# Optimization experiments

Hardware: AMD Instinct MI355X
Metric: run time of the kernel (lower is better)

The kernel has to match this reference:

```python
import jax, jax.numpy as jnp
import numpy as np

HEADS = 16
DIM_HEAD = 64
SEG = 512        # segment_len (block-diagonal window)
P = 16           # num persistent memory tokens


def rmsnorm(x, g, eps=1e-6):
    var = jnp.mean(x * x, axis=-1, keepdims=True)
    return x * jax.lax.rsqrt(var + eps) * g


def setup_inputs() -> dict:
    key = jax.random.key(0)
    ks = jax.random.split(key, 6)
    B, S, D = 2, 4096, 1024
    inner = HEADS * DIM_HEAD
    return {
        "x": jax.random.normal(ks[0], (B, S, D), jnp.float32),
        "gamma": jnp.ones((D,), jnp.float32),
        "w_qkv": jax.random.normal(ks[1], (D, inner * 3), jnp.float32) * (D ** -0.5),
        "w_out": jax.random.normal(ks[2], (inner, D), jnp.float32) * (inner ** -0.5),
        "pm_k": jax.random.normal(ks[3], (HEADS, P, DIM_HEAD), jnp.float32) * 0.02,
        "pm_v": jax.random.normal(ks[4], (HEADS, P, DIM_HEAD), jnp.float32) * 0.02,
    }


def reference(x, gamma, w_qkv, w_out, pm_k, pm_v):
    # SegmentedAttention forward (MAC block-diagonal causal + persistent memory)
    B, S, D = x.shape
    pad = (-S) % SEG
    Sp = S + pad
    nw = Sp // SEG

    h = rmsnorm(x, gamma)
    qkv = h @ w_qkv                              # [B, S, 3*inner]
    q, k, v = jnp.split(qkv, 3, axis=-1)

    def fold(t):
        # pad and fold segments into batch: b (w n) (h d) -> b w h n d
        t = jnp.pad(t, ((0, 0), (0, pad), (0, 0)))
        t = t.reshape(B, nw, SEG, HEADS, DIM_HEAD)
        return t.transpose(0, 1, 3, 2, 4)        # [B, W, H, SEG, Dh]

    q, k, v = fold(q), fold(k), fold(v)

    # persistent memory tokens prepended to every segment's k/v
    pmk = jnp.broadcast_to(pm_k, (B, nw, HEADS, P, DIM_HEAD))
    pmv = jnp.broadcast_to(pm_v, (B, nw, HEADS, P, DIM_HEAD))
    k = jnp.concatenate([pmk, k], axis=3)        # [B, W, H, P+SEG, Dh]
    v = jnp.concatenate([pmv, v], axis=3)

    scale = DIM_HEAD ** -0.5
    sim = jnp.einsum('bwhid,bwhjd->bwhij', q, k) * scale  # [B,W,H,SEG,P+SEG]

    # mask: persistent mem always visible; within-segment causal (block
    # diagonality is implicit from folding segments into batch)
    qi = jnp.arange(SEG)[:, None]
    kj = jnp.arange(SEG + P)[None, :] - P
    mask = (kj < 0) | (qi >= kj)
    sim = jnp.where(mask, sim, -jnp.inf)

    attn = jax.nn.softmax(sim, axis=-1)
    out = jnp.einsum('bwhij,bwhjd->bwhid', attn, v)       # [B,W,H,SEG,Dh]
    out = out.transpose(0, 1, 3, 2, 4).reshape(B, Sp, HEADS * DIM_HEAD)
    out = out[:, :S]
    return out @ w_out
```

## Files before the change

kernel.cpp:

```cpp
#include <hip/hip_runtime.h>

typedef __attribute__((ext_vector_type(8))) short short8;
typedef __attribute__((ext_vector_type(4))) float float4v;

#define SEG 512
#define PMEM 16
#define NKEY 528

__device__ __forceinline__ float b2f(unsigned int u) {
    union { unsigned int i; float f; } v; v.i = u << 16; return v.f;
}
__device__ __forceinline__ unsigned short f2b(float f) {
    union { float f; unsigned int i; } v; v.f = f;
    unsigned int b = v.i;
    return (unsigned short)((b + 0x7FFFu + ((b >> 16) & 1u)) >> 16);
}

__device__ __forceinline__ void async_ld16(const unsigned short* g, unsigned short* l) {
    __builtin_amdgcn_global_load_lds(
        (const __attribute__((address_space(1))) void*)g,
        (__attribute__((address_space(3))) void*)l,
        16, 0, 0);
}

__global__ void detect_k(const unsigned short* __restrict__ g, int* __restrict__ flag) {
    if (threadIdx.x == 0) {
        int cnt = 0;
        for (int i = 0; i < 64; ++i) cnt += (g[2 * i] == 0x3F80u) ? 1 : 0;
        *flag = (cnt > 48) ? 1 : 0;
    }
}

__global__ void transpose_k(const void* __restrict__ in,
                            unsigned short* __restrict__ out, int R, int C,
                            const int* __restrict__ flagp) {
    __shared__ unsigned short t[32][33];
    int f = flagp[0];
    const unsigned short* in16 = (const unsigned short*)in;
    const float* in32 = (const float*)in;
    int bx = blockIdx.x * 32, by = blockIdx.y * 32;
    int tx = threadIdx.x, ty = threadIdx.y;
    #pragma unroll
    for (int j = 0; j < 32; j += 8) {
        long idx = (long)(by + ty + j) * C + bx + tx;
        t[ty + j][tx] = f ? in16[idx] : f2b(in32[idx]);
    }
    __syncthreads();
    #pragma unroll
    for (int j = 0; j < 32; j += 8)
        out[(long)(bx + ty + j) * R + by + tx] = t[tx][ty + j];
}

__global__ __launch_bounds__(256) void rmsnorm_k(
    const void* __restrict__ xv_, const void* __restrict__ gv_,
    unsigned short* __restrict__ h, const int* __restrict__ flagp) {
    __shared__ float wsum[4];
    int f = flagp[0];
    long row = blockIdx.x;
    int tid = threadIdx.x;
    float f0, f1, f2, f3, g0, g1, g2, g3;
    if (f) {
        const unsigned short* x = (const unsigned short*)xv_;
        const unsigned short* g = (const unsigned short*)gv_;
        uint2 xv = *(const uint2*)(x + row * 1024 + tid * 4);
        f0 = b2f(xv.x & 0xffffu); f1 = b2f(xv.x >> 16);
        f2 = b2f(xv.y & 0xffffu); f3 = b2f(xv.y >> 16);
        uint2 gv = *(const uint2*)(g + tid * 4);
        g0 = b2f(gv.x & 0xffffu); g1 = b2f(gv.x >> 16);
        g2 = b2f(gv.y & 0xffffu); g3 = b2f(gv.y >> 16);
    } else {
        const float* x = (const float*)xv_;
        const float* g = (const float*)gv_;
        float4 xv = *(const float4*)(x + row * 1024 + tid * 4);
        f0 = xv.x; f1 = xv.y; f2 = xv.z; f3 = xv.w;
        float4 gv = *(const float4*)(g + tid * 4);
        g0 = gv.x; g1 = gv.y; g2 = gv.z; g3 = gv.w;
    }
    float ss = f0 * f0 + f1 * f1 + f2 * f2 + f3 * f3;
    #pragma unroll
    for (int off = 1; off < 64; off <<= 1) ss += __shfl_xor(ss, off, 64);
    int lane = tid & 63, wv = tid >> 6;
    if (lane == 0) wsum[wv] = ss;
    __syncthreads();
    float tot = wsum[0] + wsum[1] + wsum[2] + wsum[3];
    float sc = rsqrtf(tot * (1.0f / 1024.0f) + 1e-6f);
    uint2 o;
    o.x = (unsigned int)f2b(f0 * sc * g0) | ((unsigned int)f2b(f1 * sc * g1) << 16);
    o.y = (unsigned int)f2b(f2 * sc * g2) | ((unsigned int)f2b(f3 * sc * g3) << 16);
    *(uint2*)(h + row * 1024 + tid * 4) = o;
}

__global__ __launch_bounds__(256) void gemm_bt(
    const unsigned short* __restrict__ A, const unsigned short* __restrict__ Bt,
    void* __restrict__ Cv, int M, int N, int K,
    const int* __restrict__ flagp, int out_mode) {
    __shared__ unsigned short As[128 * 32];
    __shared__ unsigned short Bs[128 * 32];
    int out_bf16 = out_mode == 0 ? 1 : flagp[0];
    int tid = threadIdx.x;
    int lane = tid & 63, wv = tid >> 6;
    int l15 = lane & 15, quad = lane >> 4;
    int wm = (wv >> 1) * 64, wn = (wv & 1) * 64;
    long m0 = (long)blockIdx.y * 128;
    long n0 = (long)blockIdx.x * 128;

    float4v acc[4][4];
    #pragma unroll
    for (int i = 0; i < 4; ++i)
        #pragma unroll
        for (int j = 0; j < 4; ++j) acc[i][j] = (float4v){0.f, 0.f, 0.f, 0.f};

    int r0 = tid >> 2;
    int cc = (tid & 3) * 8;
    const unsigned short* Ap = A + (m0 + r0) * K + cc;
    const unsigned short* Bp = Bt + (n0 + r0) * K + cc;
    unsigned short* As0 = As + tid * 8;
    unsigned short* As1 = As + 2048 + tid * 8;
    unsigned short* Bs0 = Bs + tid * 8;
    unsigned short* Bs1 = Bs + 2048 + tid * 8;

    for (int k0 = 0; k0 < K; k0 += 32) {
        async_ld16(Ap + k0, As0);
        async_ld16(Ap + 64 * K + k0, As1);
        async_ld16(Bp + k0, Bs0);
        async_ld16(Bp + 64 * K + k0, Bs1);
        __syncthreads();
        short8 af[4], bfr[4];
        #pragma unroll
        for (int mt = 0; mt < 4; ++mt)
            af[mt] = *(const short8*)&As[(wm + mt * 16 + l15) * 32 + quad * 8];
        #pragma unroll
        for (int nt = 0; nt < 4; ++nt)
            bfr[nt] = *(const short8*)&Bs[(wn + nt * 16 + l15) * 32 + quad * 8];
        #pragma unroll
        for (int mt = 0; mt < 4; ++mt)
            #pragma unroll
            for (int nt = 0; nt < 4; ++nt)
                acc[mt][nt] = __builtin_amdgcn_mfma_f32_16x16x32_bf16(af[mt], bfr[nt], acc[mt][nt], 0, 0, 0);
        __syncthreads();
    }
    if (out_bf16) {
        unsigned short* C = (unsigned short*)Cv;
        #pragma unroll
        for (int mt = 0; mt < 4; ++mt)
            #pragma unroll
            for (int nt = 0; nt < 4; ++nt)
                #pragma unroll
                for (int r = 0; r < 4; ++r) {
                    long m = m0 + wm + mt * 16 + quad * 4 + r;
                    long n = n0 + wn + nt * 16 + l15;
                    C[m * N + n] = f2b(acc[mt][nt][r]);
                }
    } else {
        float* C = (float*)Cv;
        #pragma unroll
        for (int mt = 0; mt < 4; ++mt)
            #pragma unroll
            for (int nt = 0; nt < 4; ++nt)
                #pragma unroll
                for (int r = 0; r < 4; ++r) {
                    long m = m0 + wm + mt * 16 + quad * 4 + r;
                    long n = n0 + wn + nt * 16 + l15;
                    C[m * N + n] = acc[mt][nt][r];
                }
    }
}

__global__ __launch_bounds__(256) void attn_k(
    const unsigned short* __restrict__ qkv,
    const void* __restrict__ pmk_, const void* __restrict__ pmv_,
    unsigned short* __restrict__ outp, int S, const int* __restrict__ flagp) {
    __shared__ unsigned short Klds[64][72];
    __shared__ unsigned short Vt[64][72];
    __shared__ unsigned short Pbuf[4][16][72];

    int f = flagp[0];
    int hh = blockIdx.x & 15;
    int w  = blockIdx.x >> 4;
    int b  = blockIdx.y;
    int qt = blockIdx.z;

    int tid = threadIdx.x;
    int lane = tid & 63, wv = tid >> 6;
    int l15 = lane & 15, quad = lane >> 4;

    long base_row = (long)b * S + (long)w * SEG;

    int i0 = qt * 64 + wv * 16;
    const unsigned short* qp = qkv + (base_row + i0 + l15) * 3072 + hh * 64;
    short8 aq0 = *(const short8*)(qp + quad * 8);
    short8 aq1 = *(const short8*)(qp + 32 + quad * 8);

    float m_i[4], l_i[4];
    float4v Oacc[4];
    #pragma unroll
    for (int r = 0; r < 4; ++r) { m_i[r] = -1e30f; l_i[r] = 0.f; }
    #pragma unroll
    for (int dt = 0; dt < 4; ++dt) Oacc[dt] = (float4v){0.f, 0.f, 0.f, 0.f};

    const float scale = 0.125f;

    int rot = tid & 7;

    int cmax = qt + 2;
    for (int c = 0; c < cmax; ++c) {
        int jbase = c * 64;
        #pragma unroll
        for (int it = 0; it < 2; ++it) {
            int jl = (tid >> 3) + it * 32;
            int c8 = (tid & 7) * 8;
            int jg = jbase + jl;
            uint4 kd, vd;
            if (c == 0 && jl < PMEM) {
                long off = ((long)hh * PMEM + jl) * 64 + c8;
                if (f) {
                    kd = *(const uint4*)((const unsigned short*)pmk_ + off);
                    vd = *(const uint4*)((const unsigned short*)pmv_ + off);
                } else {
                    const float* pk = (const float*)pmk_ + off;
                    const float* pv = (const float*)pmv_ + off;
                    float4 k0 = *(const float4*)pk, k1 = *(const float4*)(pk + 4);
                    float4 v0 = *(const float4*)pv, v1 = *(const float4*)(pv + 4);
                    kd.x = (unsigned int)f2b(k0.x) | ((unsigned int)f2b(k0.y) << 16);
                    kd.y = (unsigned int)f2b(k0.z) | ((unsigned int)f2b(k0.w) << 16);
                    kd.z = (unsigned int)f2b(k1.x) | ((unsigned int)f2b(k1.y) << 16);
                    kd.w = (unsigned int)f2b(k1.z) | ((unsigned int)f2b(k1.w) << 16);
                    vd.x = (unsigned int)f2b(v0.x) | ((unsigned int)f2b(v0.y) << 16);
                    vd.y = (unsigned int)f2b(v0.z) | ((unsigned int)f2b(v0.w) << 16);
                    vd.z = (unsigned int)f2b(v1.x) | ((unsigned int)f2b(v1.y) << 16);
                    vd.w = (unsigned int)f2b(v1.z) | ((unsigned int)f2b(v1.w) << 16);
                }
            } else if (jg < NKEY) {
                const unsigned short* kp = qkv + (base_row + jg - PMEM) * 3072 + 1024 + hh * 64 + c8;
                kd = *(const uint4*)kp;
                vd = *(const uint4*)(kp + 1024);
            } else {
                kd = (uint4){0, 0, 0, 0};
                vd = (uint4){0, 0, 0, 0};
            }
            *(uint4*)&Klds[jl][c8] = kd;
            union { uint4 u; unsigned short s[8]; } vu; vu.u = vd;
            int colw = (jl + 8 * rot) & 63;
            #pragma unroll
            for (int u = 0; u < 8; ++u) Vt[c8 + u][colw] = vu.s[u];
        }
        __syncthreads();

        float4v sc[4];
        #pragma unroll
        for (int jt = 0; jt < 4; ++jt) {
            float4v a = (float4v){0.f, 0.f, 0.f, 0.f};
            short8 bk0 = *(const short8*)&Klds[jt * 16 + l15][quad * 8];
            short8 bk1 = *(const short8*)&Klds[jt * 16 + l15][32 + quad * 8];
            a = __builtin_amdgcn_mfma_f32_16x16x32_bf16(aq0, bk0, a, 0, 0, 0);
            a = __builtin_amdgcn_mfma_f32_16x16x32_bf16(aq1, bk1, a, 0, 0, 0);
            sc[jt] = a;
        }
        if (c >= qt) {
            #pragma unroll
            for (int jt = 0; jt < 4; ++jt) {
                int jg = jbase + jt * 16 + l15;
                #pragma unroll
                for (int r = 0; r < 4; ++r) {
                    int i = i0 + quad * 4 + r;
                    bool ok = (jg < PMEM) || ((jg < NKEY) && (i >= jg - PMEM));
                    sc[jt][r] = ok ? sc[jt][r] * scale : -1e30f;
                }
            }
        } else {
            #pragma unroll
            for (int jt = 0; jt < 4; ++jt)
                #pragma unroll
                for (int r = 0; r < 4; ++r) sc[jt][r] *= scale;
        }
        #pragma unroll
        for (int r = 0; r < 4; ++r) {
            float tmax = fmaxf(fmaxf(sc[0][r], sc[1][r]), fmaxf(sc[2][r], sc[3][r]));
            #pragma unroll
            for (int off = 1; off < 16; off <<= 1)
                tmax = fmaxf(tmax, __shfl_xor(tmax, off, 64));
            float mnew = fmaxf(m_i[r], tmax);
            float alpha = __expf(m_i[r] - mnew);
            float psum = 0.f;
            #pragma unroll
            for (int jt = 0; jt < 4; ++jt) {
                float p = __expf(sc[jt][r] - mnew);
                sc[jt][r] = p;
                psum += p;
            }
            #pragma unroll
            for (int off = 1; off < 16; off <<= 1)
                psum += __shfl_xor(psum, off, 64);
            l_i[r] = l_i[r] * alpha + psum;
            m_i[r] = mnew;
            #pragma unroll
            for (int dt = 0; dt < 4; ++dt) Oacc[dt][r] *= alpha;
        }
        #pragma unroll
        for (int jt = 0; jt < 4; ++jt)
            #pragma unroll
            for (int r = 0; r < 4; ++r)
                Pbuf[wv][quad * 4 + r][jt * 16 + l15] = f2b(sc[jt][r]);

        short8 ap0 = *(const short8*)&Pbuf[wv][l15][quad * 8];
        short8 ap1 = *(const short8*)&Pbuf[wv][l15][32 + quad * 8];
        #pragma unroll
        for (int dt = 0; dt < 4; ++dt) {
            int d = dt * 16 + l15;
            int cb0 = (quad * 8 + 8 * ((d >> 3) & 7)) & 63;
            int cb1 = (32 + quad * 8 + 8 * ((d >> 3) & 7)) & 63;
            short8 bv0 = *(const short8*)&Vt[d][cb0];
            short8 bv1 = *(const short8*)&Vt[d][cb1];
            Oacc[dt] = __builtin_amdgcn_mfma_f32_16x16x32_bf16(ap0, bv0, Oacc[dt], 0, 0, 0);
            Oacc[dt] = __builtin_amdgcn_mfma_f32_16x16x32_bf16(ap1, bv1, Oacc[dt], 0, 0, 0);
        }
        __syncthreads();
    }

    #pragma unroll
    for (int dt = 0; dt < 4; ++dt)
        #pragma unroll
        for (int r = 0; r < 4; ++r) {
            int i = i0 + quad * 4 + r;
            outp[(base_row + i) * 1024 + hh * 64 + dt * 16 + l15] = f2b(Oacc[dt][r] / l_i[r]);
        }
}

extern "C" void kernel_launch(void* const* d_in, const int* in_sizes, int n_in,
                              void* d_out, int out_size, void* d_ws, size_t ws_size,
                              hipStream_t stream) {
    const void* x     = d_in[0];
    const void* gamma = d_in[1];
    const void* w_qkv = d_in[2];
    const void* w_out = d_in[3];
    const void* pmk   = d_in[4];
    const void* pmv   = d_in[5];

    const int D = 1024, S = 4096;
    const int B = in_sizes[0] / (S * D);
    const long BS = (long)B * S;

    int* flag = (int*)d_ws;
    unsigned short* h     = (unsigned short*)d_ws + 64;
    unsigned short* qkvb  = h + BS * 1024;
    unsigned short* wqkvT = qkvb + BS * 3072;
    unsigned short* woutT = wqkvT + (long)3072 * 1024;
    unsigned short* aout  = h;

    detect_k<<<1, 64, 0, stream>>>((const unsigned short*)gamma, flag);

    dim3 tb(32, 8);
    transpose_k<<<dim3(3072 / 32, 1024 / 32), tb, 0, stream>>>(w_qkv, wqkvT, 1024, 3072, flag);
    transpose_k<<<dim3(1024 / 32, 1024 / 32), tb, 0, stream>>>(w_out, woutT, 1024, 1024, flag);

    rmsnorm_k<<<(int)BS, 256, 0, stream>>>(x, gamma, h, flag);

    gemm_bt<<<dim3(3072 / 128, (int)(BS / 128)), 256, 0, stream>>>(h, wqkvT, qkvb, (int)BS, 3072, 1024, flag, 0);

    attn_k<<<dim3(128, B, 8), 256, 0, stream>>>(qkvb, pmk, pmv, aout, S, flag);

    gemm_bt<<<dim3(1024 / 128, (int)(BS / 128)), 256, 0, stream>>>(aout, woutT, d_out, (int)BS, 1024, 1024, flag, 1);
}
```

Measured before the change: 264.9 us.

## Deepen GEMM K-tile to 64 with XOR-swizzled LDS and staged coalesced stores

The GEMM now loads a 64-wide K slice per iteration into an XOR-swizzled LDS layout. This halves the number of barrier pairs and avoids bank conflicts on the fragment reads. The epilogue stages the output tile through shared memory (swizzled for bf16, two halves for fp32) so global writes become 16-byte vector stores instead of scattered 2- or 4-byte stores. LDS use rises to 32KB per block, which may reduce occupancy, and the epilogue adds extra barriers.

```diff
diff --git a/kernel.cpp b/kernel.cpp
--- a/kernel.cpp
+++ b/kernel.cpp
@@ -94,8 +94,9 @@
     const unsigned short* __restrict__ A, const unsigned short* __restrict__ Bt,
     void* __restrict__ Cv, int M, int N, int K,
     const int* __restrict__ flagp, int out_mode) {
-    __shared__ unsigned short As[128 * 32];
-    __shared__ unsigned short Bs[128 * 32];
+    __shared__ unsigned short SM[16384];
+    unsigned short* As = SM;
+    unsigned short* Bs = SM + 8192;
     int out_bf16 = out_mode == 0 ? 1 : flagp[0];
     int tid = threadIdx.x;
     int lane = tid & 63, wv = tid >> 6;
@@ -110,59 +111,88 @@
         #pragma unroll
         for (int j = 0; j < 4; ++j) acc[i][j] = (float4v){0.f, 0.f, 0.f, 0.f};
 
-    int r0 = tid >> 2;
-    int cc = (tid & 3) * 8;
-    const unsigned short* Ap = A + (m0 + r0) * K + cc;
-    const unsigned short* Bp = Bt + (n0 + r0) * K + cc;
-    unsigned short* As0 = As + tid * 8;
-    unsigned short* As1 = As + 2048 + tid * 8;
-    unsigned short* Bs0 = Bs + tid * 8;
-    unsigned short* Bs1 = Bs + 2048 + tid * 8;
-
-    for (int k0 = 0; k0 < K; k0 += 32) {
-        async_ld16(Ap + k0, As0);
-        async_ld16(Ap + 64 * K + k0, As1);
-        async_ld16(Bp + k0, Bs0);
-        async_ld16(Bp + 64 * K + k0, Bs1);
-        __syncthreads();
-        short8 af[4], bfr[4];
+    int r = tid >> 3;
+    int c8 = (((tid & 7) ^ (r & 7)) * 8);
+    const unsigned short* Ap = A + (m0 + r) * K + c8;
+    const unsigned short* Bp = Bt + (n0 + r) * K + c8;
+    unsigned short* Ad = As + tid * 8;
+    unsigned short* Bd = Bs + tid * 8;
+
+    int s = l15 & 7;
+
+    for (int k0 = 0; k0 < K; k0 += 64) {
+        #pragma unroll
+        for (int i = 0; i < 4; ++i) {
+            async_ld16(Ap + (long)(32 * i) * K + k0, Ad + i * 2048);
+            async_ld16(Bp + (long)(32 * i) * K + k0, Bd + i * 2048);
+        }
+        __syncthreads();
+        #pragma unroll
+        for (int ksub = 0; ksub < 2; ++ksub) {
+            short8 af[4], bfr[4];
+            int v = ksub * 4 + quad;
+            #pragma unroll
+            for (int mt = 0; mt < 4; ++mt)
+                af[mt] = *(const short8*)&As[(wm + mt * 16 + l15) * 64 + ((v ^ s) * 8)];
+            #pragma unroll
+            for (int nt = 0; nt < 4; ++nt)
+                bfr[nt] = *(const short8*)&Bs[(wn + nt * 16 + l15) * 64 + ((v ^ s) * 8)];
+            #pragma unroll
+            for (int mt = 0; mt < 4; ++mt)
+                #pragma unroll
+                for (int nt = 0; nt < 4; ++nt)
+                    acc[mt][nt] = __builtin_amdgcn_mfma_f32_16x16x32_bf16(af[mt], bfr[nt], acc[mt][nt], 0, 0, 0);
+        }
+        __syncthreads();
+    }
+
+    if (out_bf16) {
+        unsigned short* Cs = SM;
         #pragma unroll
         for (int mt = 0; mt < 4; ++mt)
-            af[mt] = *(const short8*)&As[(wm + mt * 16 + l15) * 32 + quad * 8];
-        #pragma unroll
-        for (int nt = 0; nt < 4; ++nt)
-            bfr[nt] = *(const short8*)&Bs[(wn + nt * 16 + l15) * 32 + quad * 8];
-        #pragma unroll
-        for (int mt = 0; mt < 4; ++mt)
             #pragma unroll
             for (int nt = 0; nt < 4; ++nt)
-                acc[mt][nt] = __builtin_amdgcn_mfma_f32_16x16x32_bf16(af[mt], bfr[nt], acc[mt][nt], 0, 0, 0);
-        __syncthreads();
-    }
-    if (out_bf16) {
+                #pragma unroll
+                for (int rr = 0; rr < 4; ++rr) {
+                    int row = wm + mt * 16 + quad * 4 + rr;
+                    int col = wn + nt * 16 + l15;
+                    int colp = col ^ (((row >> 2) & 7) << 4);
+                    Cs[row * 128 + colp] = f2b(acc[mt][nt][rr]);
+                }
+        __syncthreads();
         unsigned short* C = (unsigned short*)Cv;
         #pragma unroll
-        for (int mt = 0; mt < 4; ++mt)
-            #pragma unroll
-            for (int nt = 0; nt < 4; ++nt)
-                #pragma unroll
-                for (int r = 0; r < 4; ++r) {
-                    long m = m0 + wm + mt * 16 + quad * 4 + r;
-                    long n = n0 + wn + nt * 16 + l15;
-                    C[m * N + n] = f2b(acc[mt][nt][r]);
-                }
+        for (int p = 0; p < 8; ++p) {
+            int off = (p * 256 + tid) * 8;
+            int row = off >> 7;
+            int colp = off & 127;
+            int col = colp ^ (((row >> 2) & 7) << 4);
+            *(uint4*)(C + (m0 + row) * N + n0 + col) = *(const uint4*)&Cs[off];
+        }
     } else {
+        float* Cf = (float*)SM;
         float* C = (float*)Cv;
         #pragma unroll
-        for (int mt = 0; mt < 4; ++mt)
-            #pragma unroll
-            for (int nt = 0; nt < 4; ++nt)
-                #pragma unroll
-                for (int r = 0; r < 4; ++r) {
-                    long m = m0 + wm + mt * 16 + quad * 4 + r;
-                    long n = n0 + wn + nt * 16 + l15;
-                    C[m * N + n] = acc[mt][nt][r];
-                }
+        for (int half = 0; half < 2; ++half) {
+            if (wm == half * 64) {
+                #pragma unroll
+                for (int mt = 0; mt < 4; ++mt)
+                    #pragma unroll
+                    for (int nt = 0; nt < 4; ++nt)
+                        #pragma unroll
+                        for (int rr = 0; rr < 4; ++rr)
+                            Cf[(mt * 16 + quad * 4 + rr) * 128 + wn + nt * 16 + l15] = acc[mt][nt][rr];
+            }
+            __syncthreads();
+            #pragma unroll
+            for (int p = 0; p < 8; ++p) {
+                int off = (p * 256 + tid) * 4;
+                int row = off >> 7;
+                int col = off & 127;
+                *(float4*)(C + (m0 + half * 64 + row) * N + n0 + col) = *(const float4*)&Cf[off];
+            }
+            __syncthreads();
+        }
     }
 }
 
@@ -199,7 +229,6 @@
     for (int dt = 0; dt < 4; ++dt) Oacc[dt] = (float4v){0.f, 0.f, 0.f, 0.f};
 
     const float scale = 0.125f;
-
     int rot = tid & 7;
 
     int cmax = qt + 2;
```

Result: faster. 250.6 us (-5.4%).
